# Optimization experiments

Measured on AMD Instinct MI355X. Metric: run time of the kernel, lower is better.

Reference implementation:

```python
import jax, jax.numpy as jnp
import numpy as np
from jax import lax


def _conv(x, w, b):
    out = lax.conv_general_dilated(x, w, (1, 1), [(0, 0), (0, 0)],
                                   dimension_numbers=('NCHW', 'OIHW', 'NCHW'))
    return out + b[None, :, None, None]


def _bn(x, g, b, eps=1e-5):
    # BatchNorm2d in training mode: biased batch statistics over (N,H,W)
    m = jnp.mean(x, axis=(0, 2, 3), keepdims=True)
    v = jnp.var(x, axis=(0, 2, 3), keepdims=True)
    return (x - m) * lax.rsqrt(v + eps) * g[None, :, None, None] + b[None, :, None, None]


def _maxpool2(x):
    return lax.reduce_window(x, -jnp.inf, lax.max, (1, 1, 2, 2), (1, 1, 2, 2), 'VALID')


def _topk_mask(x, k):
    # TopK module: keep the k largest-|.| channels per (b,h,w), zero the rest.
    a = jnp.abs(x)
    kth = lax.top_k(jnp.moveaxis(a, 1, -1), k)[0][..., -1]  # [B,H,W] k-th largest |x|
    return x * (a >= kth[:, None, :, :]).astype(x.dtype)


def _embiggen(x):
    # im2col 3x3 stride 1 valid, flattened channel-major (c, kh, kw) like
    # patch.contiguous().view(B,-1) in the torch loop, but fully vectorized.
    B, C, H, W = x.shape
    Ho, Wo = H - 2, W - 2
    patches = jnp.stack([x[:, :, i:i + Ho, j:j + Wo]
                         for i in range(3) for j in range(3)], axis=2)  # [B,C,9,Ho,Wo]
    return patches.reshape(B, C * 9, Ho, Wo)


def setup_inputs() -> dict:
    key = jax.random.key(0)
    ks = jax.random.split(key, 40)
    it = iter(range(40))

    def w(shape):
        fan_in = int(np.prod(shape[1:]))
        return (jax.random.normal(ks[next(it)], shape, jnp.float32)
                / np.float32(np.sqrt(fan_in)))

    def bias(n):
        return jax.random.normal(ks[next(it)], (n,), jnp.float32) * 0.01

    def gamma(n):
        return jax.random.uniform(ks[next(it)], (n,), jnp.float32, 0.5, 1.5)

    inp = {}
    inp['x'] = jax.random.normal(ks[next(it)], (256, 3, 32, 32), jnp.float32)
    inp['enc_w'] = w((256, 3, 3, 3)); inp['enc_b'] = bias(256)
    inp['dec_w'] = w((27, 256, 1, 1)); inp['dec_b'] = bias(27)
    inp['red_w'] = w((64, 256, 1, 1)); inp['red_b'] = bias(64)
    inp['bn1_g'] = gamma(64); inp['bn1_b'] = bias(64)
    inp['conv1_w'] = w((96, 64, 3, 3)); inp['conv1_b'] = bias(96)
    inp['bn2_g'] = gamma(96); inp['bn2_b'] = bias(96)
    inp['conv2_w'] = w((128, 96, 3, 3)); inp['conv2_b'] = bias(128)
    inp['bn3_g'] = gamma(128); inp['bn3_b'] = bias(128)
    inp['conv3_w'] = w((160, 128, 3, 3)); inp['conv3_b'] = bias(160)
    inp['bn4_g'] = gamma(160); inp['bn4_b'] = bias(160)
    inp['conv4_w'] = w((192, 160, 3, 3)); inp['conv4_b'] = bias(192)
    inp['bn5_g'] = gamma(192); inp['bn5_b'] = bias(192)
    inp['conv5_w'] = w((256, 192, 3, 3)); inp['conv5_b'] = bias(256)
    inp['bnc_g'] = gamma(256); inp['bnc_b'] = bias(256)
    inp['fc_w'] = w((100, 1024)); inp['fc_b'] = bias(100)
    inp['k'] = 32  # round(64 / k_div=2)
    return inp


def reference(x, enc_w, enc_b, dec_w, dec_b, red_w, red_b,
              bn1_g, bn1_b, conv1_w, conv1_b,
              bn2_g, bn2_b, conv2_w, conv2_b,
              bn3_g, bn3_b, conv3_w, conv3_b,
              bn4_g, bn4_b, conv4_w, conv4_b,
              bn5_g, bn5_b, conv5_w, conv5_b,
              bnc_g, bnc_b, fc_w, fc_b, k):
    # SparseCodingLayer_First (encoder+topk computed once; torch recomputes identically)
    s = _topk_mask(_conv(x, enc_w, enc_b), k)            # [B,256,30,30]
    dec = jax.nn.sigmoid(_conv(s, dec_w, dec_b))         # [B,27,30,30]
    target = lax.stop_gradient(_embiggen(x))             # detached im2col target
    aux_loss = jnp.mean((target - dec) ** 2)
    h = _conv(s, red_w, red_b)                           # [B,64,30,30]
    # Conv6 backbone
    h = _maxpool2(_conv(jax.nn.relu(_bn(h, bn1_g, bn1_b)), conv1_w, conv1_b))  # [B,96,14,14]
    h = _conv(jax.nn.relu(_bn(h, bn2_g, bn2_b)), conv2_w, conv2_b)             # [B,128,12,12]
    h = _conv(jax.nn.relu(_bn(h, bn3_g, bn3_b)), conv3_w, conv3_b)             # [B,160,10,10]
    h = _maxpool2(_conv(jax.nn.relu(_bn(h, bn4_g, bn4_b)), conv4_w, conv4_b))  # [B,192,4,4]
    h = _conv(jax.nn.relu(_bn(h, bn5_g, bn5_b)), conv5_w, conv5_b)             # [B,256,2,2]
    feat = lax.stop_gradient(h)  # usecase == 'pretrain': features detached
    f = _bn(feat, bnc_g, bnc_b).reshape(feat.shape[0], -1)  # [B,1024]
    logits = f @ fc_w.T + fc_b                               # [B,100]
    preds = jnp.argmax(logits, axis=1)
    return logits, preds, aux_loss
```

## Files before the change

kernel.cpp:

```cpp
#include <hip/hip_runtime.h>

#define DEV_INLINE __device__ __forceinline__
typedef unsigned long long ull;
typedef unsigned int u32;
typedef unsigned short u16;
typedef __attribute__((ext_vector_type(8))) short short8v;
typedef __attribute__((ext_vector_type(4))) float f32x4;

DEV_INLINE u32 rne16(float f){
  u32 u = __float_as_uint(f);
  return (u + 0x7fffu + ((u>>16)&1u)) >> 16;
}
DEV_INLINE u32 packsplit(float a){
  u32 h = rne16(a);
  float hf = __uint_as_float(h<<16);
  u32 l = rne16(a - hf);
  return h | (l<<16);
}
DEV_INLINE float unpackv(u32 w){
  return __uint_as_float(w<<16) + __uint_as_float(w & 0xffff0000u);
}

__global__ void prep_all(const float* __restrict__ enc_w, float* __restrict__ encTg,
                         const float* __restrict__ dec_w, float* __restrict__ decT,
                         const float* __restrict__ red_w, float* __restrict__ redT,
                         const float* __restrict__ fc_w,  float* __restrict__ fcT,
                         const float* __restrict__ c1w, u16* __restrict__ W1h, u16* __restrict__ W1l,
                         const float* __restrict__ c2w, u16* __restrict__ W2h, u16* __restrict__ W2l,
                         const float* __restrict__ c3w, u16* __restrict__ W3h, u16* __restrict__ W3l,
                         const float* __restrict__ c4w, u16* __restrict__ W4h, u16* __restrict__ W4l,
                         const float* __restrict__ c5w, u16* __restrict__ W5h, u16* __restrict__ W5l)
{
  const int b = blockIdx.x, t = threadIdx.x;
  auto t2 = [&](const float* A, float* AT, int R, int C, int base){
    int i = (b-base)*256 + t; if (i < R*C){ int r=i%R, c=i/R; AT[i] = A[r*C+c]; }
  };
  auto pk = [&](const float* W, u16* wh, u16* wl, int CIN, int COUT, int base){
    int TPI = CIN/32, KS = 9*TPI;
    int tid = (b-base)*256 + t;
    if (tid >= KS*COUT) return;
    int co = tid % COUT, ks = tid / COUT;
    int tap = ks/TPI, cib = (ks - tap*TPI)*32;
    u16* dh = wh + (size_t)tid*32;
    u16* dl = wl + (size_t)tid*32;
    for (int kl=0; kl<32; ++kl){
      float w = W[((size_t)(co*CIN + cib + kl))*9 + tap];
      u32 h = rne16(w);
      float hf = __uint_as_float(h<<16);
      u32 l = rne16(w - hf);
      dh[kl] = (u16)h; dl[kl] = (u16)l;
    }
  };
  if      (b < 27)  t2(enc_w, encTg, 256, 27, 0);
  else if (b < 54)  t2(dec_w, decT, 27, 256, 27);
  else if (b < 118) t2(red_w, redT, 64, 256, 54);
  else if (b < 518) t2(fc_w,  fcT, 100, 1024, 118);
  else if (b < 525) pk(c1w, W1h, W1l, 64, 96, 518);
  else if (b < 539) pk(c2w, W2h, W2l, 96, 128, 525);
  else if (b < 562) pk(c3w, W3h, W3l, 128, 160, 539);
  else if (b < 596) pk(c4w, W4h, W4l, 160, 192, 562);
  else              pk(c5w, W5h, W5l, 192, 256, 596);
}

__global__ __launch_bounds__(256, 4) void stage_a1(
    const float* __restrict__ encTg, const float* __restrict__ enc_b,
    const float* __restrict__ x, const int* __restrict__ kp,
    float* __restrict__ svg_v, unsigned char* __restrict__ svg_i)
{
  __shared__ float  rows[9*32];
  __shared__ float  svf[30*33];
  __shared__ unsigned char svi[30*33];

  const int t = threadIdx.x, oh = blockIdx.x, b = blockIdx.y;
  const int k = __builtin_amdgcn_readfirstlane(*kp);
  const int wid = t>>6, lane = t&63;
  const float4* encW4 = (const float4*)encTg;

  for (int e=t; e<288; e+=256){
    int ci = e/96, r = (e/32)%3, xx = e&31;
    rows[(ci*3+r)*32+xx] = x[((b*3+ci)*32 + (oh+r))*32 + xx];
  }
  for (int e=t; e<990; e+=256){ svf[e]=0.f; svi[e]=0; }
  __syncthreads();

  const float4 eb = ((const float4*)enc_b)[lane];

  auto cnt4 = [&](unsigned c, unsigned u0, unsigned u1, unsigned u2, unsigned u3)->int{
    return __popcll(__ballot(u0>=c)) + __popcll(__ballot(u1>=c))
         + __popcll(__ballot(u2>=c)) + __popcll(__ballot(u3>=c));
  };
  auto compact = [&](float v0,float v1,float v2,float v3,
                     unsigned u0,unsigned u1,unsigned u2,unsigned u3,
                     unsigned th, int pi){
    bool k0=u0>=th, k1=u1>=th, k2=u2>=th, k3=u3>=th;
    ull B0=__ballot(k0), B1=__ballot(k1), B2=__ballot(k2), B3=__ballot(k3);
    ull below=(1ull<<lane)-1ull;
    int n0=__popcll(B0), n1=__popcll(B1), n2=__popcll(B2);
    int o0=__popcll(B0&below);
    int o1=n0+__popcll(B1&below);
    int o2=n0+n1+__popcll(B2&below);
    int o3=n0+n1+n2+__popcll(B3&below);
    float* sf = &svf[pi*33]; unsigned char* si = &svi[pi*33];
    if (k0&&o0<32){ sf[o0]=v0; si[o0]=(unsigned char)(4*lane+0); }
    if (k1&&o1<32){ sf[o1]=v1; si[o1]=(unsigned char)(4*lane+1); }
    if (k2&&o2<32){ sf[o2]=v2; si[o2]=(unsigned char)(4*lane+2); }
    if (k3&&o3<32){ sf[o3]=v3; si[o3]=(unsigned char)(4*lane+3); }
  };

  for (int it=0; it<4; ++it){
    const int pr = wid*4 + it;
    if (pr >= 15) break;
    const int ow0 = 2*pr;

    float a0=eb.x,a1=eb.y,a2=eb.z,a3=eb.w;
    float c0=eb.x,c1=eb.y,c2=eb.z,c3=eb.w;
    #pragma unroll
    for (int ci=0; ci<3; ++ci)
      #pragma unroll
      for (int i=0;i<3;++i){
        const int rbase = (ci*3+i)*32 + ow0;
        float p0 = rows[rbase+0], p1 = rows[rbase+1];
        float p2 = rows[rbase+2], p3 = rows[rbase+3];
        float4 w0 = encW4[(ci*9+i*3+0)*64 + lane];
        float4 w1 = encW4[(ci*9+i*3+1)*64 + lane];
        float4 w2 = encW4[(ci*9+i*3+2)*64 + lane];
        a0=fmaf(w0.x,p0,a0); a1=fmaf(w0.y,p0,a1); a2=fmaf(w0.z,p0,a2); a3=fmaf(w0.w,p0,a3);
        c0=fmaf(w0.x,p1,c0); c1=fmaf(w0.y,p1,c1); c2=fmaf(w0.z,p1,c2); c3=fmaf(w0.w,p1,c3);
        a0=fmaf(w1.x,p1,a0); a1=fmaf(w1.y,p1,a1); a2=fmaf(w1.z,p1,a2); a3=fmaf(w1.w,p1,a3);
        c0=fmaf(w1.x,p2,c0); c1=fmaf(w1.y,p2,c1); c2=fmaf(w1.z,p2,c2); c3=fmaf(w1.w,p2,c3);
        a0=fmaf(w2.x,p2,a0); a1=fmaf(w2.y,p2,a1); a2=fmaf(w2.z,p2,a2); a3=fmaf(w2.w,p2,a3);
        c0=fmaf(w2.x,p3,c0); c1=fmaf(w2.y,p3,c1); c2=fmaf(w2.z,p3,c2); c3=fmaf(w2.w,p3,c3);
      }

    unsigned A0=__float_as_uint(a0)&0x7fffffffu, A1=__float_as_uint(a1)&0x7fffffffu;
    unsigned A2=__float_as_uint(a2)&0x7fffffffu, A3=__float_as_uint(a3)&0x7fffffffu;
    unsigned C0=__float_as_uint(c0)&0x7fffffffu, C1=__float_as_uint(c1)&0x7fffffffu;
    unsigned C2=__float_as_uint(c2)&0x7fffffffu, C3=__float_as_uint(c3)&0x7fffffffu;

    unsigned thA=0, thB=0;
    int dA=0, dB=0;
    for (int bit=30; bit>=0; --bit){
      if (!dA){
        unsigned c = thA | (1u<<bit);
        int n = cnt4(c,A0,A1,A2,A3);
        if (n>=k) thA=c;
        if (n==k) dA=1;
      }
      if (!dB){
        unsigned c = thB | (1u<<bit);
        int n = cnt4(c,C0,C1,C2,C3);
        if (n>=k) thB=c;
        if (n==k) dB=1;
      }
      if (dA & dB) break;
    }

    compact(a0,a1,a2,a3, A0,A1,A2,A3, thA, ow0);
    compact(c0,c1,c2,c3, C0,C1,C2,C3, thB, ow0+1);
  }
  __syncthreads();

  const size_t gbase = (size_t)b*900 + (size_t)oh*30;
  for (int e=t; e<960; e+=256){
    int jj = e/30, pi = e - jj*30;
    svg_v[(size_t)jj*230400 + gbase + pi] = svf[pi*33+jj];
    svg_i[(size_t)jj*230400 + gbase + pi] = svi[pi*33+jj];
  }
}

__global__ __launch_bounds__(256, 2) void stage_a2(
    const float* __restrict__ svg_v, const unsigned char* __restrict__ svg_i,
    const float* __restrict__ decT, const float* __restrict__ dec_b,
    const float* __restrict__ x, float* __restrict__ auxp)
{
  __shared__ __align__(16) float decl[256*28];
  __shared__ float redbuf[256];
  const int t = threadIdx.x;
  for (int e=t; e<6912; e+=256){
    int r = e/27, o = e - r*27;
    decl[r*28+o] = decT[e];
  }
  __syncthreads();

  const int pos = blockIdx.x*256 + t;
  const int b = pos/900, rem = pos - b*900;
  const int oh = rem/30, ow = rem - (rem/30)*30;

  float d[27];
  #pragma unroll
  for (int o=0;o<27;++o) d[o] = dec_b[o];
  for (int jj=0; jj<32; ++jj){
    float v  = svg_v[(size_t)jj*230400 + pos];
    int  idx = (int)svg_i[(size_t)jj*230400 + pos];
    const float4* wr4 = (const float4*)(decl + idx*28);
    float4 w0=wr4[0], w1=wr4[1], w2=wr4[2], w3=wr4[3], w4=wr4[4], w5=wr4[5], w6=wr4[6];
    d[0]=fmaf(v,w0.x,d[0]);  d[1]=fmaf(v,w0.y,d[1]);  d[2]=fmaf(v,w0.z,d[2]);  d[3]=fmaf(v,w0.w,d[3]);
    d[4]=fmaf(v,w1.x,d[4]);  d[5]=fmaf(v,w1.y,d[5]);  d[6]=fmaf(v,w1.z,d[6]);  d[7]=fmaf(v,w1.w,d[7]);
    d[8]=fmaf(v,w2.x,d[8]);  d[9]=fmaf(v,w2.y,d[9]);  d[10]=fmaf(v,w2.z,d[10]); d[11]=fmaf(v,w2.w,d[11]);
    d[12]=fmaf(v,w3.x,d[12]); d[13]=fmaf(v,w3.y,d[13]); d[14]=fmaf(v,w3.z,d[14]); d[15]=fmaf(v,w3.w,d[15]);
    d[16]=fmaf(v,w4.x,d[16]); d[17]=fmaf(v,w4.y,d[17]); d[18]=fmaf(v,w4.z,d[18]); d[19]=fmaf(v,w4.w,d[19]);
    d[20]=fmaf(v,w5.x,d[20]); d[21]=fmaf(v,w5.y,d[21]); d[22]=fmaf(v,w5.z,d[22]); d[23]=fmaf(v,w5.w,d[23]);
    d[24]=fmaf(v,w6.x,d[24]); d[25]=fmaf(v,w6.y,d[25]); d[26]=fmaf(v,w6.z,d[26]);
  }
  float acc = 0.f;
  #pragma unroll
  for (int o=0;o<27;++o){
    int ci = o/9, r2 = (o - ci*9)/3, c2 = o%3;
    float tg = x[((b*3+ci)*32 + (oh+r2))*32 + (ow+c2)];
    float dv = 1.f/(1.f + __expf(-d[o]));
    float df = tg - dv;
    acc = fmaf(df, df, acc);
  }
  redbuf[t]=acc; __syncthreads();
  for (int off=128; off; off>>=1){ if (t<off) redbuf[t]+=redbuf[t+off]; __syncthreads(); }
  if (t==0) auxp[blockIdx.x] = redbuf[0];
}

__global__ __launch_bounds__(256) void stage_a3p2(
    const float* __restrict__ svg_v, const unsigned char* __restrict__ svg_i,
    const float* __restrict__ redT, const float* __restrict__ red_b,
    u32* __restrict__ x1p, float* __restrict__ psum1, float* __restrict__ psq1)
{
  __shared__ __align__(16) float redl[256*68];
  __shared__ u32   obuf[256*65];
  const int t = threadIdx.x;
  for (int e=t; e<16384; e+=256) redl[(e>>6)*68 + (e&63)] = redT[e];
  __syncthreads();

  const int pos = blockIdx.x*256 + t;

  float v[32]; int a[32];
  #pragma unroll
  for (int j=0;j<32;++j) v[j] = svg_v[(size_t)j*230400 + pos];
  #pragma unroll
  for (int j=0;j<32;++j) a[j] = (int)svg_i[(size_t)j*230400 + pos]*17;

  const float4* redl4 = (const float4*)redl;
  #pragma unroll 2
  for (int ocb=0; ocb<16; ++ocb){
    float s0 = red_b[4*ocb+0], s1 = red_b[4*ocb+1];
    float s2 = red_b[4*ocb+2], s3 = red_b[4*ocb+3];
    #pragma unroll
    for (int j=0;j<32;++j){
      float4 w = redl4[a[j] + ocb];
      s0 = fmaf(v[j], w.x, s0); s1 = fmaf(v[j], w.y, s1);
      s2 = fmaf(v[j], w.z, s2); s3 = fmaf(v[j], w.w, s3);
    }
    obuf[t*65 + 4*ocb+0] = packsplit(s0);
    obuf[t*65 + 4*ocb+1] = packsplit(s1);
    obuf[t*65 + 4*ocb+2] = packsplit(s2);
    obuf[t*65 + 4*ocb+3] = packsplit(s3);
  }
  __syncthreads();

  const size_t base = (size_t)blockIdx.x*16384;
  float s = 0.f, q = 0.f;
  for (int e=t; e<16384; e+=256){
    u32 w = obuf[(e>>6)*65 + (e&63)];
    x1p[base + e] = w;
    float vv = unpackv(w);
    s += vv; q = fmaf(vv, vv, q);
  }
  float* ls = redl; float* lq = redl + 256;
  ls[t] = s; lq[t] = q; __syncthreads();
  if (t < 128){ ls[t] += ls[t+128]; lq[t] += lq[t+128]; } __syncthreads();
  if (t < 64){
    psum1[(size_t)blockIdx.x*64 + t] = ls[t] + ls[t+64];
    psq1 [(size_t)blockIdx.x*64 + t] = lq[t] + lq[t+64];
  }
}

template<int C>
__global__ __launch_bounds__(256) void bn_finalG(
    const float* __restrict__ ps, const float* __restrict__ pq, int G,
    const float* __restrict__ g, const float* __restrict__ b2,
    float* __restrict__ sc, float* __restrict__ sh, float inv_n)
{
  __shared__ float ls[256], lq[256];
  const int c = blockIdx.x, t = threadIdx.x;
  float s=0.f, q=0.f;
  for (int i=t; i<G; i+=256){ s += ps[(size_t)i*C+c]; q += pq[(size_t)i*C+c]; }
  ls[t]=s; lq[t]=q; __syncthreads();
  for (int off=128; off; off>>=1){
    if (t<off){ ls[t]+=ls[t+off]; lq[t]+=lq[t+off]; } __syncthreads();
  }
  if (t==0){
    float m = ls[0]*inv_n;
    float var = fmaf(lq[0], inv_n, -m*m);
    float rs = rsqrtf(var + 1e-5f);
    float scale = g[c]*rs;
    sc[c] = scale;
    sh[c] = fmaf(-m, scale, b2[c]);
  }
}

__global__ __launch_bounds__(256) void bn1_final(
    const float* __restrict__ ps, const float* __restrict__ pq,
    const float* __restrict__ g, const float* __restrict__ b2,
    float* __restrict__ sc, float* __restrict__ sh)
{
  __shared__ float ls[256], lq[256];
  const int c = blockIdx.x, t = threadIdx.x;
  float s=0.f, q=0.f;
  for (int i=t; i<900; i+=256){ s += ps[(size_t)i*64+c]; q += pq[(size_t)i*64+c]; }
  ls[t]=s; lq[t]=q; __syncthreads();
  for (int off=128; off; off>>=1){
    if (t<off){ ls[t]+=ls[t+off]; lq[t]+=lq[t+off]; } __syncthreads();
  }
  if (t==0){
    constexpr float inv_n = 1.f/230400.f;
    float m = ls[0]*inv_n;
    float var = fmaf(lq[0], inv_n, -m*m);
    float rs = rsqrtf(var + 1e-5f);
    float scale = g[c]*rs;
    sc[c] = scale;
    sh[c] = fmaf(-m, scale, b2[c]);
  }
}

template<int C>
__global__ void cvt_repack(u32* __restrict__ xp, const float* __restrict__ sc,
                           const float* __restrict__ sh, int total4){
  int i = blockIdx.x*256 + threadIdx.x;
  if (i >= total4) return;
  uint4* p = (uint4*)xp;
  uint4 w = p[i];
  int cb = (i*4) % C;
  w.x = packsplit(fmaxf(fmaf(unpackv(w.x), sc[cb+0], sh[cb+0]), 0.f));
  w.y = packsplit(fmaxf(fmaf(unpackv(w.y), sc[cb+1], sh[cb+1]), 0.f));
  w.z = packsplit(fmaxf(fmaf(unpackv(w.z), sc[cb+2], sh[cb+2]), 0.f));
  w.w = packsplit(fmaxf(fmaf(unpackv(w.w), sc[cb+3], sh[cb+3]), 0.f));
  p[i] = w;
}

template<int CIN,int COUT,int HIN,int WIN,int BM,int MW,bool POOL,bool PKOUT>
__global__ __launch_bounds__(256) void conv_mfma(
    const u32* __restrict__ xp, const u16* __restrict__ wh,
    const u16* __restrict__ wl, const float* __restrict__ bias,
    void* __restrict__ y_, float* __restrict__ psC, float* __restrict__ qsC)
{
  constexpr int HC=HIN-2, WC=WIN-2, TPI=CIN/32, KS=9*TPI, NCH=COUT/16;
  const int t = threadIdx.x, wid = t>>6, lane = t&63;
  const int p0 = blockIdx.x*BM;
  const int colg = lane>>4;
  const int col = lane&15;
  float* yf = (float*)y_;
  u32*   yp = (u32*)y_;

  const u32* Aptr[MW];
  #pragma unroll
  for (int m=0;m<MW;++m){
    int l = (wid*MW+m)*16 + col;
    int lc = l < BM ? l : BM-1;
    int p = p0 + lc;
    int b = p/(HC*WC); int rem = p - b*(HC*WC);
    int oh = rem/WC, ow = rem - (rem/WC)*WC;
    Aptr[m] = xp + ((size_t)((b*HIN+oh)*WIN+ow))*CIN + colg*8;
  }
  const size_t wb = (size_t)col*32 + colg*8;

  f32x4 acc[MW][NCH];
  #pragma unroll
  for (int m=0;m<MW;++m)
    #pragma unroll
    for (int nc=0;nc<NCH;++nc) acc[m][nc] = (f32x4){0.f,0.f,0.f,0.f};

  for (int ks=0; ks<KS; ++ks){
    const int tap = ks/TPI, cib = (ks - tap*TPI)*32;
    const int kh = tap/3, kw = tap - kh*3;
    short8v ah[MW], al[MW];
    #pragma unroll
    for (int m=0;m<MW;++m){
      const u32* ap = Aptr[m] + (kh*WIN + kw)*CIN + cib;
      uint4 qa = *(const uint4*)(ap);
      uint4 qb = *(const uint4*)(ap+4);
      ah[m][0]=(short)(qa.x&0xffffu); al[m][0]=(short)(qa.x>>16);
      ah[m][1]=(short)(qa.y&0xffffu); al[m][1]=(short)(qa.y>>16);
      ah[m][2]=(short)(qa.z&0xffffu); al[m][2]=(short)(qa.z>>16);
      ah[m][3]=(short)(qa.w&0xffffu); al[m][3]=(short)(qa.w>>16);
      ah[m][4]=(short)(qb.x&0xffffu); al[m][4]=(short)(qb.x>>16);
      ah[m][5]=(short)(qb.y&0xffffu); al[m][5]=(short)(qb.y>>16);
      ah[m][6]=(short)(qb.z&0xffffu); al[m][6]=(short)(qb.z>>16);
      ah[m][7]=(short)(qb.w&0xffffu); al[m][7]=(short)(qb.w>>16);
    }
    const u16* whp = wh + (size_t)ks*COUT*32 + wb;
    const u16* wlp = wl + (size_t)ks*COUT*32 + wb;
    #pragma unroll
    for (int nc=0;nc<NCH;++nc){
      short8v bh = *(const short8v*)(whp + nc*512);
      short8v bl = *(const short8v*)(wlp + nc*512);
      #pragma unroll
      for (int m=0;m<MW;++m){
        acc[m][nc] = __builtin_amdgcn_mfma_f32_16x16x32_bf16(ah[m], bh, acc[m][nc], 0,0,0);
        acc[m][nc] = __builtin_amdgcn_mfma_f32_16x16x32_bf16(ah[m], bl, acc[m][nc], 0,0,0);
        acc[m][nc] = __builtin_amdgcn_mfma_f32_16x16x32_bf16(al[m], bh, acc[m][nc], 0,0,0);
      }
    }
  }

  if constexpr (!POOL){
    __shared__ float ldsS[4][COUT], ldsQ[4][COUT];
    float sacc[NCH], qacc[NCH];
    #pragma unroll
    for (int nc=0;nc<NCH;++nc){ sacc[nc]=0.f; qacc[nc]=0.f; }
    #pragma unroll
    for (int m=0;m<MW;++m){
      const int lr0 = (wid*MW+m)*16 + colg*4;
      #pragma unroll
      for (int nc=0;nc<NCH;++nc){
        float bv = bias[nc*16+col];
        #pragma unroll
        for (int r=0;r<4;++r)
          if (lr0+r < BM){
            float ov = acc[m][nc][r] + bv;
            float vv;
            if constexpr (PKOUT){
              u32 w = packsplit(ov);
              yp[(size_t)(p0+lr0+r)*COUT + nc*16+col] = w;
              vv = unpackv(w);
            } else {
              yf[(size_t)(p0+lr0+r)*COUT + nc*16+col] = ov;
              vv = ov;
            }
            sacc[nc] += vv; qacc[nc] = fmaf(vv, vv, qacc[nc]);
          }
      }
    }
    #pragma unroll
    for (int nc=0;nc<NCH;++nc){
      float s_ = sacc[nc], q_ = qacc[nc];
      s_ += __shfl_xor(s_, 16); q_ += __shfl_xor(q_, 16);
      s_ += __shfl_xor(s_, 32); q_ += __shfl_xor(q_, 32);
      if (colg == 0){ ldsS[wid][nc*16+col] = s_; ldsQ[wid][nc*16+col] = q_; }
    }
    __syncthreads();
    if (t < COUT){
      psC[(size_t)blockIdx.x*COUT + t] = ldsS[0][t]+ldsS[1][t]+ldsS[2][t]+ldsS[3][t];
      qsC[(size_t)blockIdx.x*COUT + t] = ldsQ[0][t]+ldsQ[1][t]+ldsQ[2][t]+ldsQ[3][t];
    }
  } else {
    constexpr int LDC = COUT+4;
    __shared__ float lds[BM*LDC];
    #pragma unroll
    for (int m=0;m<MW;++m){
      const int lr0 = (wid*MW+m)*16 + colg*4;
      #pragma unroll
      for (int nc=0;nc<NCH;++nc){
        float bv = bias[nc*16+col];
        #pragma unroll
        for (int r=0;r<4;++r)
          if (lr0+r < BM) lds[(lr0+r)*LDC + nc*16+col] = acc[m][nc][r] + bv;
      }
    }
    __syncthreads();
    constexpr int WPO = WC/2;
    const size_t pbase = (size_t)p0/4;
    if (t < COUT){
      float s = 0.f, q = 0.f;
      for (int pl=0; pl<BM/4; ++pl){
        int poh = pl / WPO, pw = pl - poh*WPO;
        int r = (2*poh)*WC + 2*pw;
        float mx = fmaxf(fmaxf(lds[r*LDC+t],      lds[(r+1)*LDC+t]),
                         fmaxf(lds[(r+WC)*LDC+t], lds[(r+WC+1)*LDC+t]));
        float vv;
        if constexpr (PKOUT){
          u32 w = packsplit(mx);
          yp[(pbase + pl)*COUT + t] = w;
          vv = unpackv(w);
        } else {
          yf[(pbase + pl)*COUT + t] = mx;
          vv = mx;
        }
        s += vv; q = fmaf(vv, vv, q);
      }
      psC[(size_t)blockIdx.x*COUT + t] = s;
      qsC[(size_t)blockIdx.x*COUT + t] = q;
    }
  }
}

__global__ __launch_bounds__(256) void fc_kernel(
    const float* __restrict__ a5, const float* __restrict__ scale, const float* __restrict__ shift,
    const float* __restrict__ fcT, const float* __restrict__ fc_b,
    const float* __restrict__ auxp, float* __restrict__ outp)
{
  const int b = blockIdx.x, t = threadIdx.x;
  if (b == 256){
    __shared__ float s[256];
    float a=0.f;
    for (int i=t; i<900; i+=256) a += auxp[i];
    s[t]=a; __syncthreads();
    for (int off=128; off; off>>=1){ if (t<off) s[t]+=s[t+off]; __syncthreads(); }
    if (t==0) outp[25856] = s[0] / 6220800.0f;
    return;
  }
  __shared__ float f[1024];
  __shared__ float part[256];
  __shared__ float lg[128];
  for (int e=t; e<1024; e+=256){
    int c = e & 255, hw = e >> 8;
    float v = a5[b*1024 + e];
    f[c*4 + hw] = fmaf(v, scale[c], shift[c]);
  }
  __syncthreads();
  const int o = t & 127, half = t >> 7;
  float s = 0.f;
  if (o < 100){
    const float* fp = f + half*512;
    const float* wp = fcT + half*512*100 + o;
    for (int j=0;j<512;++j) s = fmaf(fp[j], wp[j*100], s);
  }
  part[t] = s; __syncthreads();
  if (t < 128){
    float logit = part[t] + part[t+128] + ((t<100)? fc_b[t] : 0.f);
    lg[t] = (t<100)? logit : -3.0e38f;
    if (t<100) outp[b*100 + t] = logit;
  }
  __syncthreads();
  if (t==0){
    float m = lg[0]; int mi = 0;
    for (int i=1;i<100;++i){ if (lg[i] > m){ m = lg[i]; mi = i; } }
    outp[25600 + b] = (float)mi;
  }
}

extern "C" void kernel_launch(void* const* d_in, const int* in_sizes, int n_in,
                              void* d_out, int out_size, void* d_ws, size_t ws_size,
                              hipStream_t stream)
{
  (void)in_sizes; (void)n_in; (void)out_size;
  const float* x     = (const float*)d_in[0];
  const float* enc_w = (const float*)d_in[1];
  const float* enc_b = (const float*)d_in[2];
  const float* dec_w = (const float*)d_in[3];
  const float* dec_b = (const float*)d_in[4];
  const float* red_w = (const float*)d_in[5];
  const float* red_b = (const float*)d_in[6];
  const float* bn1_g = (const float*)d_in[7];  const float* bn1_b = (const float*)d_in[8];
  const float* c1w   = (const float*)d_in[9];  const float* c1b   = (const float*)d_in[10];
  const float* bn2_g = (const float*)d_in[11]; const float* bn2_b = (const float*)d_in[12];
  const float* c2w   = (const float*)d_in[13]; const float* c2b   = (const float*)d_in[14];
  const float* bn3_g = (const float*)d_in[15]; const float* bn3_b = (const float*)d_in[16];
  const float* c3w   = (const float*)d_in[17]; const float* c3b   = (const float*)d_in[18];
  const float* bn4_g = (const float*)d_in[19]; const float* bn4_b = (const float*)d_in[20];
  const float* c4w   = (const float*)d_in[21]; const float* c4b   = (const float*)d_in[22];
  const float* bn5_g = (const float*)d_in[23]; const float* bn5_b = (const float*)d_in[24];
  const float* c5w   = (const float*)d_in[25]; const float* c5b   = (const float*)d_in[26];
  const float* bnc_g = (const float*)d_in[27]; const float* bnc_b = (const float*)d_in[28];
  const float* fc_w  = (const float*)d_in[29]; const float* fc_b  = (const float*)d_in[30];
  const int*   kp    = (const int*)d_in[31];
  float* out = (float*)d_out;
  float* ws  = (float*)d_ws;

  constexpr size_t OFF_ENCT = 0;
  constexpr size_t OFF_DECT = 7168;
  constexpr size_t OFF_REDT = 14336;
  constexpr size_t OFF_FCT  = 30720;
  constexpr size_t OFF_W1H = 133120, OFF_W1L = 160768;
  constexpr size_t OFF_W2H = 188416, OFF_W2L = 243712;
  constexpr size_t OFF_W3H = 299008, OFF_W3L = 391168;
  constexpr size_t OFF_W4H = 483328, OFF_W4L = 621568;
  constexpr size_t OFF_W5H = 759808, OFF_W5L = 980992;
  constexpr size_t OFF_SS1 = 1202176, OFF_SS2 = 1202304, OFF_SS3 = 1202496;
  constexpr size_t OFF_SS4 = 1202752, OFF_SS5 = 1203072, OFF_SSC = 1203456;
  constexpr size_t OFF_AUX  = 1302272;
  constexpr size_t OFF_B    = 1303296;
  constexpr size_t OFF_C    = 16048896;
  constexpr size_t OFF_P1S  = 25264896;
  constexpr size_t OFF_P1Q  = OFF_P1S + 57600;
  constexpr size_t OFF_PCS  = OFF_P1Q + 57600;
  constexpr size_t OFF_PCQ  = OFF_PCS + 172032;
  constexpr size_t TOTALF   = OFF_PCQ + 172032;
  if (ws_size < TOTALF*sizeof(float)) return;

  float* encTg = ws + OFF_ENCT;
  float* decT = ws + OFF_DECT; float* redT = ws + OFF_REDT; float* fcT = ws + OFF_FCT;
  u16* W1h = (u16*)(ws+OFF_W1H); u16* W1l = (u16*)(ws+OFF_W1L);
  u16* W2h = (u16*)(ws+OFF_W2H); u16* W2l = (u16*)(ws+OFF_W2L);
  u16* W3h = (u16*)(ws+OFF_W3H); u16* W3l = (u16*)(ws+OFF_W3L);
  u16* W4h = (u16*)(ws+OFF_W4H); u16* W4l = (u16*)(ws+OFF_W4L);
  u16* W5h = (u16*)(ws+OFF_W5H); u16* W5l = (u16*)(ws+OFF_W5L);
  float* ss1 = ws+OFF_SS1; float* ss2 = ws+OFF_SS2; float* ss3 = ws+OFF_SS3;
  float* ss4 = ws+OFF_SS4; float* ss5 = ws+OFF_SS5; float* ssc = ws+OFF_SSC;
  float* auxp = ws+OFF_AUX;
  float* psum1 = ws+OFF_P1S; float* psq1 = ws+OFF_P1Q;
  float* pcs = ws+OFF_PCS;  float* pcq = ws+OFF_PCQ;
  u32*   x1p = (u32*)(ws+OFF_B);
  u32*   y2p = (u32*)(ws+OFF_B);
  u32*   p4p = (u32*)(ws+OFF_B);
  float* svv = ws+OFF_C;
  unsigned char* svi = (unsigned char*)(ws+OFF_C+7372800);
  u32*   p1p = (u32*)(ws+OFF_C);
  u32*   y3p = (u32*)(ws+OFF_C);
  float* y5  = ws+OFF_C;

  prep_all<<<650, 256, 0, stream>>>(enc_w, encTg, dec_w, decT, red_w, redT, fc_w, fcT,
                                    c1w, W1h, W1l, c2w, W2h, W2l, c3w, W3h, W3l,
                                    c4w, W4h, W4l, c5w, W5h, W5l);

  stage_a1<<<dim3(30,256), 256, 0, stream>>>(encTg, enc_b, x, kp, svv, svi);
  stage_a2<<<900, 256, 0, stream>>>(svv, svi, decT, dec_b, x, auxp);
  stage_a3p2<<<900, 256, 0, stream>>>(svv, svi, redT, red_b, x1p, psum1, psq1);

  bn1_final<<<64, 256, 0, stream>>>(psum1, psq1, bn1_g, bn1_b, ss1, ss1+64);
  cvt_repack<64><<<14400, 256, 0, stream>>>(x1p, ss1, ss1+64, 3686400);

  conv_mfma<64,96,30,30,112,2,true,true><<<1792, 256, 0, stream>>>(x1p, W1h, W1l, c1b, p1p, pcs, pcq);
  bn_finalG<96><<<96, 256, 0, stream>>>(pcs, pcq, 1792, bn2_g, bn2_b, ss2, ss2+96, 1.f/50176.f);
  cvt_repack<96><<<(1204224+255)/256, 256, 0, stream>>>(p1p, ss2, ss2+96, 1204224);

  conv_mfma<96,128,14,14,128,2,false,true><<<288, 256, 0, stream>>>(p1p, W2h, W2l, c2b, y2p, pcs, pcq);
  bn_finalG<128><<<128, 256, 0, stream>>>(pcs, pcq, 288, bn3_g, bn3_b, ss3, ss3+128, 1.f/36864.f);
  cvt_repack<128><<<(1179648+255)/256, 256, 0, stream>>>(y2p, ss3, ss3+128, 1179648);

  conv_mfma<128,160,12,12,128,2,false,true><<<200, 256, 0, stream>>>(y2p, W3h, W3l, c3b, y3p, pcs, pcq);
  bn_finalG<160><<<160, 256, 0, stream>>>(pcs, pcq, 200, bn4_g, bn4_b, ss4, ss4+160, 1.f/25600.f);
  cvt_repack<160><<<(1024000+255)/256, 256, 0, stream>>>(y3p, ss4, ss4+160, 1024000);

  conv_mfma<160,192,10,10,64,1,true,true><<<256, 256, 0, stream>>>(y3p, W4h, W4l, c4b, p4p, pcs, pcq);
  bn_finalG<192><<<192, 256, 0, stream>>>(pcs, pcq, 256, bn5_g, bn5_b, ss5, ss5+192, 1.f/4096.f);
  cvt_repack<192><<<(196608+255)/256, 256, 0, stream>>>(p4p, ss5, ss5+192, 196608);

  conv_mfma<192,256,4,4,64,1,false,false><<<16, 256, 0, stream>>>(p4p, W5h, W5l, c5b, y5, pcs, pcq);
  bn_finalG<256><<<256, 256, 0, stream>>>(pcs, pcq, 16, bnc_g, bnc_b, ssc, ssc+256, 1.f/1024.f);
  fc_kernel<<<257, 256, 0, stream>>>(y5, ssc, ssc+256, fcT, fc_b, auxp, out);
}
```

Baseline: 1.114 ms.

## Drop LDS staging in red conv and move BN1 stats to a separate pass

```diff
diff --git a/kernel.cpp b/kernel.cpp
--- a/kernel.cpp
+++ b/kernel.cpp
@@ -216,13 +216,12 @@
   if (t==0) auxp[blockIdx.x] = redbuf[0];
 }
 
-__global__ __launch_bounds__(256) void stage_a3p2(
+__global__ __launch_bounds__(256) void stage_a3p3(
     const float* __restrict__ svg_v, const unsigned char* __restrict__ svg_i,
     const float* __restrict__ redT, const float* __restrict__ red_b,
-    u32* __restrict__ x1p, float* __restrict__ psum1, float* __restrict__ psq1)
+    u32* __restrict__ x1p)
 {
   __shared__ __align__(16) float redl[256*68];
-  __shared__ u32   obuf[256*65];
   const int t = threadIdx.x;
   for (int e=t; e<16384; e+=256) redl[(e>>6)*68 + (e&63)] = redT[e];
   __syncthreads();
@@ -236,6 +235,7 @@
   for (int j=0;j<32;++j) a[j] = (int)svg_i[(size_t)j*230400 + pos]*17;
 
   const float4* redl4 = (const float4*)redl;
+  uint4* outp = (uint4*)(x1p + (size_t)pos*64);
   #pragma unroll 2
   for (int ocb=0; ocb<16; ++ocb){
     float s0 = red_b[4*ocb+0], s1 = red_b[4*ocb+1];
@@ -246,27 +246,25 @@
       s0 = fmaf(v[j], w.x, s0); s1 = fmaf(v[j], w.y, s1);
       s2 = fmaf(v[j], w.z, s2); s3 = fmaf(v[j], w.w, s3);
     }
-    obuf[t*65 + 4*ocb+0] = packsplit(s0);
-    obuf[t*65 + 4*ocb+1] = packsplit(s1);
-    obuf[t*65 + 4*ocb+2] = packsplit(s2);
-    obuf[t*65 + 4*ocb+3] = packsplit(s3);
-  }
-  __syncthreads();
-
-  const size_t base = (size_t)blockIdx.x*16384;
-  float s = 0.f, q = 0.f;
-  for (int e=t; e<16384; e+=256){
-    u32 w = obuf[(e>>6)*65 + (e&63)];
-    x1p[base + e] = w;
-    float vv = unpackv(w);
-    s += vv; q = fmaf(vv, vv, q);
-  }
-  float* ls = redl; float* lq = redl + 256;
-  ls[t] = s; lq[t] = q; __syncthreads();
-  if (t < 128){ ls[t] += ls[t+128]; lq[t] += lq[t+128]; } __syncthreads();
-  if (t < 64){
-    psum1[(size_t)blockIdx.x*64 + t] = ls[t] + ls[t+64];
-    psq1 [(size_t)blockIdx.x*64 + t] = lq[t] + lq[t+64];
+    outp[ocb] = (uint4){packsplit(s0), packsplit(s1), packsplit(s2), packsplit(s3)};
+  }
+}
+
+__global__ __launch_bounds__(256) void bn1_partial(
+    const u32* __restrict__ in, float* __restrict__ psum, float* __restrict__ psq)
+{
+  const int t = threadIdx.x, c = t&63, g = t>>6;
+  float s=0.f, q=0.f;
+  for (int i = blockIdx.x*4 + g; i < 230400; i += 768){
+    float v = unpackv(in[(size_t)i*64 + c]);
+    s += v; q = fmaf(v, v, q);
+  }
+  __shared__ float ls[256], lq[256];
+  ls[t]=s; lq[t]=q; __syncthreads();
+  if (t<128){ ls[t]+=ls[t+128]; lq[t]+=lq[t+128]; } __syncthreads();
+  if (t<64){
+    psum[(size_t)blockIdx.x*64 + t] = ls[t] + ls[t+64];
+    psq [(size_t)blockIdx.x*64 + t] = lq[t] + lq[t+64];
   }
 }
 
@@ -285,30 +283,6 @@
     if (t<off){ ls[t]+=ls[t+off]; lq[t]+=lq[t+off]; } __syncthreads();
   }
   if (t==0){
-    float m = ls[0]*inv_n;
-    float var = fmaf(lq[0], inv_n, -m*m);
-    float rs = rsqrtf(var + 1e-5f);
-    float scale = g[c]*rs;
-    sc[c] = scale;
-    sh[c] = fmaf(-m, scale, b2[c]);
-  }
-}
-
-__global__ __launch_bounds__(256) void bn1_final(
-    const float* __restrict__ ps, const float* __restrict__ pq,
-    const float* __restrict__ g, const float* __restrict__ b2,
-    float* __restrict__ sc, float* __restrict__ sh)
-{
-  __shared__ float ls[256], lq[256];
-  const int c = blockIdx.x, t = threadIdx.x;
-  float s=0.f, q=0.f;
-  for (int i=t; i<900; i+=256){ s += ps[(size_t)i*64+c]; q += pq[(size_t)i*64+c]; }
-  ls[t]=s; lq[t]=q; __syncthreads();
-  for (int off=128; off; off>>=1){
-    if (t<off){ ls[t]+=ls[t+off]; lq[t]+=lq[t+off]; } __syncthreads();
-  }
-  if (t==0){
-    constexpr float inv_n = 1.f/230400.f;
     float m = ls[0]*inv_n;
     float var = fmaf(lq[0], inv_n, -m*m);
     float rs = rsqrtf(var + 1e-5f);
@@ -600,9 +574,10 @@
 
   stage_a1<<<dim3(30,256), 256, 0, stream>>>(encTg, enc_b, x, kp, svv, svi);
   stage_a2<<<900, 256, 0, stream>>>(svv, svi, decT, dec_b, x, auxp);
-  stage_a3p2<<<900, 256, 0, stream>>>(svv, svi, redT, red_b, x1p, psum1, psq1);
-
-  bn1_final<<<64, 256, 0, stream>>>(psum1, psq1, bn1_g, bn1_b, ss1, ss1+64);
+  stage_a3p3<<<900, 256, 0, stream>>>(svv, svi, redT, red_b, x1p);
+
+  bn1_partial<<<192, 256, 0, stream>>>(x1p, psum1, psq1);
+  bn_finalG<64><<<64, 256, 0, stream>>>(psum1, psq1, 192, bn1_g, bn1_b, ss1, ss1+64, 1.f/230400.f);
   cvt_repack<64><<<14400, 256, 0, stream>>>(x1p, ss1, ss1+64, 3686400);
 
   conv_mfma<64,96,30,30,112,2,true,true><<<1792, 256, 0, stream>>>(x1p, W1h, W1l, c1b, p1p, pcs, pcq);
```

Result: slower. 1.169 ms (+4.9%).
